# Kernel tuning notes

Measured on AMD Instinct MI355X. Metric: run time of the kernel, lower is better.

Reference implementation:

```python
import jax, jax.numpy as jnp
import numpy as np

D = 1024
HS = 64
NH = D // HS


def setup_inputs() -> dict:
    key = jax.random.key(0)
    ks = jax.random.split(key, 8)
    B, S = 2, 2048
    x = jax.random.normal(ks[0], (B, S, D), dtype=jnp.float32)
    y = jax.random.normal(ks[1], (B, S, D), dtype=jnp.float32)
    pad_mask = jax.random.randint(ks[2], (B, S), 0, 2).astype(jnp.int32)
    sc = 1.0 / np.sqrt(D)
    Wq = jax.random.normal(ks[3], (D, D), dtype=jnp.float32) * sc
    Wk = jax.random.normal(ks[4], (D, D), dtype=jnp.float32) * sc
    Wv = jax.random.normal(ks[5], (D, D), dtype=jnp.float32) * sc
    Wp = jax.random.normal(ks[6], (D, D), dtype=jnp.float32) * sc
    bp = jnp.zeros((D,), dtype=jnp.float32)
    return {"x": x, "y": y, "pad_mask": pad_mask, "Wq": Wq, "Wk": Wk, "Wv": Wv, "Wp": Wp, "bp": bp}


def reference(x, y, pad_mask, Wq, Wk, Wv, Wp, bp):
    B, S, _ = x.shape
    # torch Linear: out = in @ W.T  (bias=False for q/k/v)
    q = (y @ Wq.T).reshape(B, S, NH, HS).transpose(0, 2, 1, 3)  # [B,H,S,hs]
    k = (x @ Wk.T).reshape(B, S, NH, HS).transpose(0, 2, 1, 3)
    v = (x @ Wv.T).reshape(B, S, NH, HS).transpose(0, 2, 1, 3)
    att = jnp.einsum('bhqd,bhkd->bhqk', q, k) * (HS ** -0.5)  # [B,H,S,S]
    att = jnp.where((pad_mask == 0)[:, None, None, :], -jnp.inf, att)
    att = jax.nn.softmax(att, axis=-1)
    out = jnp.einsum('bhqk,bhkd->bhqd', att, v)  # [B,H,S,hs]
    out = out.transpose(0, 2, 1, 3).reshape(B, S, D)
    return out @ Wp.T + bp
```

## Files before the change

kernel.cpp:

```cpp
#include <hip/hip_runtime.h>
#include <hip/hip_bf16.h>
#include <stdint.h>

typedef unsigned short u16;
typedef unsigned int u32;
typedef float __attribute__((ext_vector_type(4))) f32x4;
typedef __bf16 __attribute__((ext_vector_type(8))) bfrag;

#define DEV static __device__ __forceinline__

DEV u16 f2bf(float f) {
  union { float f; u32 u; } c; c.f = f;
  u32 u = c.u;
  u += 0x7fffu + ((u >> 16) & 1u);
  return (u16)(u >> 16);
}

DEV u16 bf16bits(float f) {
  __hip_bfloat16 h = __float2bfloat16(f);
  return *reinterpret_cast<u16*>(&h);
}

typedef const u32 __attribute__((address_space(1)))* gas_t;
typedef u32 __attribute__((address_space(3)))* las_t;

DEV void async16(const void* g, void* l) {
  __builtin_amdgcn_global_load_lds((gas_t)(uintptr_t)g, (las_t)(uintptr_t)l, 16, 0, 0);
}

__global__ __launch_bounds__(256) void convert_all(
    const float* __restrict__ x, const float* __restrict__ y,
    const float* __restrict__ wq, const float* __restrict__ wk,
    const float* __restrict__ wv, const float* __restrict__ wp,
    u16* __restrict__ xb, u16* __restrict__ yb,
    u16* __restrict__ wqb, u16* __restrict__ wkb,
    u16* __restrict__ wvb, u16* __restrict__ wpb) {
  const int NX4 = (2 * 2048 * 1024) / 4;
  const int NW4 = (1024 * 1024) / 4;
  const int total = 2 * NX4 + 4 * NW4;
  for (int i = blockIdx.x * blockDim.x + threadIdx.x; i < total;
       i += gridDim.x * blockDim.x) {
    const float4* s; ushort4* d; int off;
    if (i < NX4) { s = (const float4*)x; d = (ushort4*)xb; off = i; }
    else if (i < 2 * NX4) { s = (const float4*)y; d = (ushort4*)yb; off = i - NX4; }
    else {
      int k = i - 2 * NX4; int wsel = k >> 18; off = k & (NW4 - 1);
      s = (const float4*)(wsel == 0 ? wq : wsel == 1 ? wk : wsel == 2 ? wv : wp);
      d = (ushort4*)(wsel == 0 ? wqb : wsel == 1 ? wkb : wsel == 2 ? wvb : wpb);
    }
    float4 v = s[off];
    ushort4 o; o.x = f2bf(v.x); o.y = f2bf(v.y); o.z = f2bf(v.z); o.w = f2bf(v.w);
    d[off] = o;
  }
}

__global__ __launch_bounds__(256, 3) void gemm_qkv(
    const u16* __restrict__ xb, const u16* __restrict__ yb,
    const u16* __restrict__ wqb, const u16* __restrict__ wkb,
    const u16* __restrict__ wvb,
    u16* __restrict__ Qb, u16* __restrict__ Kb2, u16* __restrict__ Vtb) {
  const int Kd = 1024, Nd = 1024;
  __shared__ __align__(16) u16 Als[128 * 32];
  __shared__ __align__(16) u16 Bls[128 * 32];
  __shared__ __align__(16) u16 Tls[4][64 * 72];

  const int gid = blockIdx.x;
  const int seg = gid >> 8;
  const int bb = gid & 255;
  const int m0 = (bb >> 3) * 128, n0 = (bb & 7) * 128;
  const u16* A  = (seg == 0) ? yb : xb;
  const u16* Bw = (seg == 0) ? wqb : (seg == 1 ? wkb : wvb);

  const int t = threadIdx.x;
  const int lane = t & 63, w = t >> 6;
  const int wr = w >> 1, wc = w & 1;
  const int r15 = lane & 15, g = lane >> 4;
  const int rs = t >> 2, sg = t & 3;

  f32x4 acc[4][4] = {{}};
  const u16* ga = A + (size_t)(m0 + rs) * Kd + sg * 8;
  const u16* gb = Bw + (size_t)(n0 + rs) * Kd + sg * 8;

  for (int k0 = 0; k0 < Kd; k0 += 32) {
    async16(ga + k0, &Als[t * 8]);
    async16(ga + 64 * Kd + k0, &Als[(t + 256) * 8]);
    async16(gb + k0, &Bls[t * 8]);
    async16(gb + 64 * Kd + k0, &Bls[(t + 256) * 8]);
    __syncthreads();
    bfrag af[4], bfr[4];
#pragma unroll
    for (int i = 0; i < 4; i++)
      af[i] = *(const bfrag*)&Als[(wr * 64 + i * 16 + r15) * 32 + g * 8];
#pragma unroll
    for (int i = 0; i < 4; i++)
      bfr[i] = *(const bfrag*)&Bls[(wc * 64 + i * 16 + r15) * 32 + g * 8];
#pragma unroll
    for (int i = 0; i < 4; i++)
#pragma unroll
      for (int j = 0; j < 4; j++)
        acc[i][j] = __builtin_amdgcn_mfma_f32_16x16x32_bf16(af[i], bfr[j], acc[i][j], 0, 0, 0);
    __syncthreads();
  }

  if (seg < 2) {
    u16* C = (seg == 0) ? Qb : Kb2;
    const float scale = (seg == 0) ? 0.125f : 1.0f;
#pragma unroll
    for (int i = 0; i < 4; i++) {
#pragma unroll
      for (int j = 0; j < 4; j++) {
        int col = n0 + wc * 64 + j * 16 + r15;
        int row = m0 + wr * 64 + i * 16 + g * 4;
#pragma unroll
        for (int r = 0; r < 4; r++)
          C[(size_t)(row + r) * Nd + col] = f2bf(acc[i][j][r] * scale);
      }
    }
  } else {
#pragma unroll
    for (int i = 0; i < 4; i++)
#pragma unroll
      for (int j = 0; j < 4; j++)
#pragma unroll
        for (int r = 0; r < 4; r++)
          Tls[w][(j * 16 + r15) * 72 + (i * 16 + g * 4 + r)] = f2bf(acc[i][j][r]);
#pragma unroll
    for (int it = 0; it < 8; ++it) {
      int slot = lane + it * 64;
      int nl = slot >> 3, sgm = slot & 7;
      int4 vrow = *(const int4*)&Tls[w][nl * 72 + sgm * 8];
      int col = n0 + wc * 64 + nl;
      int h = col >> 6, hs = col & 63;
      int rowg = m0 + wr * 64 + sgm * 8;
      int b = rowg >> 11, s = rowg & 2047;
      *(int4*)&Vtb[(((size_t)b * 16 + h) * 64 + hs) * 2048 + s] = vrow;
    }
  }
}

__global__ __launch_bounds__(256, 3) void gemm_proj(
    const u16* __restrict__ A, const u16* __restrict__ Bw,
    float* __restrict__ C, const float* __restrict__ bias) {
  const int Kd = 1024, Nd = 1024;
  __shared__ __align__(16) u16 Als[128 * 32];
  __shared__ __align__(16) u16 Bls[128 * 32];
  const int t = threadIdx.x;
  const int lane = t & 63, w = t >> 6;
  const int wr = w >> 1, wc = w & 1;
  const int r15 = lane & 15, g = lane >> 4;
  const int m0 = blockIdx.y * 128, n0 = blockIdx.x * 128;
  const int rs = t >> 2, sg = t & 3;

  f32x4 acc[4][4] = {{}};
  const u16* ga = A + (size_t)(m0 + rs) * Kd + sg * 8;
  const u16* gb = Bw + (size_t)(n0 + rs) * Kd + sg * 8;

  for (int k0 = 0; k0 < Kd; k0 += 32) {
    async16(ga + k0, &Als[t * 8]);
    async16(ga + 64 * Kd + k0, &Als[(t + 256) * 8]);
    async16(gb + k0, &Bls[t * 8]);
    async16(gb + 64 * Kd + k0, &Bls[(t + 256) * 8]);
    __syncthreads();
    bfrag af[4], bfr[4];
#pragma unroll
    for (int i = 0; i < 4; i++)
      af[i] = *(const bfrag*)&Als[(wr * 64 + i * 16 + r15) * 32 + g * 8];
#pragma unroll
    for (int i = 0; i < 4; i++)
      bfr[i] = *(const bfrag*)&Bls[(wc * 64 + i * 16 + r15) * 32 + g * 8];
#pragma unroll
    for (int i = 0; i < 4; i++)
#pragma unroll
      for (int j = 0; j < 4; j++)
        acc[i][j] = __builtin_amdgcn_mfma_f32_16x16x32_bf16(af[i], bfr[j], acc[i][j], 0, 0, 0);
    __syncthreads();
  }

#pragma unroll
  for (int i = 0; i < 4; i++) {
#pragma unroll
    for (int j = 0; j < 4; j++) {
      int col = n0 + wc * 64 + j * 16 + r15;
      int row = m0 + wr * 64 + i * 16 + g * 4;
      float bv = bias[col];
#pragma unroll
      for (int r = 0; r < 4; r++)
        C[(size_t)(row + r) * Nd + col] = acc[i][j][r] + bv;
    }
  }
}

__global__ __launch_bounds__(256, 4) void attn_fwd(
    const u16* __restrict__ Q, const u16* __restrict__ Kb,
    const u16* __restrict__ Vt, const int* __restrict__ mask,
    u16* __restrict__ O) {
  __shared__ __align__(16) u16 Kls[64 * 64];
  __shared__ __align__(16) u16 Vls[64 * 64];
  __shared__ __align__(16) u16 Pls[4][16 * 64];
  __shared__ float biasl[64];

  const int bid = blockIdx.x;
  const int swz = (bid & 7) * 128 + (bid >> 3);
  const int qblk = swz & 31, bh = swz >> 5;
  const int b = bh >> 4, h = bh & 15;
  const int t = threadIdx.x, lane = t & 63, w = t >> 6;
  const int r15 = lane & 15, g = lane >> 4;
  const int qbase = qblk * 64 + w * 16;

  bfrag aQ[2];
  {
    const u16* Qg = Q + ((size_t)b * 2048 + qbase) * 1024 + h * 64;
#pragma unroll
    for (int ks = 0; ks < 2; ++ks)
      aQ[ks] = *(const bfrag*)&Qg[(size_t)r15 * 1024 + ks * 32 + g * 8];
  }

  f32x4 oacc[4] = {{}};
  float lrow[4] = {0.f, 0.f, 0.f, 0.f};

  const u16* Kg = Kb + (size_t)b * 2048 * 1024 + h * 64;
  const u16* Vg = Vt + (size_t)bh * 64 * 2048;
  const int* mg = mask + b * 2048;

  const int kr = t >> 2, kc = (t & 3) * 16;
  const int swr = (kr & 7) << 3;
  const int rdx = (r15 & 7) << 3;
  int4 nk0, nk1, nv0, nv1; float nbias = 0.f;

  auto stage_load = [&](int kv0) {
    nk0 = *(const int4*)&Kg[(size_t)(kv0 + kr) * 1024 + kc];
    nk1 = *(const int4*)&Kg[(size_t)(kv0 + kr) * 1024 + kc + 8];
    nv0 = *(const int4*)&Vg[(size_t)kr * 2048 + kv0 + kc];
    nv1 = *(const int4*)&Vg[(size_t)kr * 2048 + kv0 + kc + 8];
    if (t < 64) nbias = mg[kv0 + t] ? 0.f : -1e30f;
  };
  auto stage_write = [&]() {
    *(int4*)&Kls[kr * 64 + (kc ^ swr)] = nk0;
    *(int4*)&Kls[kr * 64 + ((kc + 8) ^ swr)] = nk1;
    *(int4*)&Vls[kr * 64 + (kc ^ swr)] = nv0;
    *(int4*)&Vls[kr * 64 + ((kc + 8) ^ swr)] = nv1;
    if (t < 64) biasl[t] = nbias;
  };

  stage_load(0);
  stage_write();
  __syncthreads();

  for (int kt = 0; kt < 32; ++kt) {
    if (kt < 31) stage_load((kt + 1) * 64);

    f32x4 sc[4] = {{}};
#pragma unroll
    for (int ks = 0; ks < 2; ++ks) {
      const int cb = (ks * 32 + g * 8) ^ rdx;
#pragma unroll
      for (int nf = 0; nf < 4; ++nf) {
        bfrag bK = *(const bfrag*)&Kls[(nf * 16 + r15) * 64 + cb];
        sc[nf] = __builtin_amdgcn_mfma_f32_16x16x32_bf16(aQ[ks], bK, sc[nf], 0, 0, 0);
      }
    }

    float bcol[4];
#pragma unroll
    for (int nf = 0; nf < 4; ++nf) bcol[nf] = biasl[nf * 16 + r15];

#pragma unroll
    for (int i = 0; i < 4; i++) {
      const int prow = g * 4 + i;
      const int pxr = (prow & 7) << 3;
      u16* pr = &Pls[w][prow * 64];
      float s = 0.f;
#pragma unroll
      for (int nf = 0; nf < 4; ++nf) {
        float p = __expf(sc[nf][i] + bcol[nf]);
        s += p;
        pr[(nf * 16 + r15) ^ pxr] = bf16bits(p);
      }
      lrow[i] += s;
    }

#pragma unroll
    for (int ks = 0; ks < 2; ++ks) {
      const int cb = (ks * 32 + g * 8) ^ rdx;
      bfrag aP = *(const bfrag*)&Pls[w][r15 * 64 + cb];
#pragma unroll
      for (int nf = 0; nf < 4; ++nf) {
        bfrag bV = *(const bfrag*)&Vls[(nf * 16 + r15) * 64 + cb];
        oacc[nf] = __builtin_amdgcn_mfma_f32_16x16x32_bf16(aP, bV, oacc[nf], 0, 0, 0);
      }
    }

    __syncthreads();
    if (kt < 31) {
      stage_write();
      __syncthreads();
    }
  }

#pragma unroll
  for (int i = 0; i < 4; i++) {
    float s = lrow[i];
    s += __shfl_xor(s, 1);
    s += __shfl_xor(s, 2);
    s += __shfl_xor(s, 4);
    s += __shfl_xor(s, 8);
    lrow[i] = s;
  }

  u16* Og = O + ((size_t)b * 2048 + qbase) * 1024 + h * 64;
#pragma unroll
  for (int i = 0; i < 4; i++) {
    float rl = 1.f / lrow[i];
    size_t ro = (size_t)(g * 4 + i) * 1024;
#pragma unroll
    for (int nf = 0; nf < 4; ++nf)
      Og[ro + nf * 16 + r15] = f2bf(oacc[nf][i] * rl);
  }
}

extern "C" void kernel_launch(void* const* d_in, const int* in_sizes, int n_in,
                              void* d_out, int out_size, void* d_ws, size_t ws_size,
                              hipStream_t stream) {
  const float* x  = (const float*)d_in[0];
  const float* y  = (const float*)d_in[1];
  const int*  msk = (const int*)d_in[2];
  const float* Wq = (const float*)d_in[3];
  const float* Wk = (const float*)d_in[4];
  const float* Wv = (const float*)d_in[5];
  const float* Wp = (const float*)d_in[6];
  const float* bp = (const float*)d_in[7];

  char* ws = (char*)d_ws;
  const size_t SZ_XB = (size_t)2 * 2048 * 1024 * 2;
  const size_t SZ_W  = (size_t)1024 * 1024 * 2;
  u16* xb  = (u16*)(ws);
  u16* yb  = (u16*)(ws + SZ_XB);
  u16* wqb = (u16*)(ws + 2 * SZ_XB);
  u16* wkb = (u16*)(ws + 2 * SZ_XB + SZ_W);
  u16* wvb = (u16*)(ws + 2 * SZ_XB + 2 * SZ_W);
  u16* wpb = (u16*)(ws + 2 * SZ_XB + 3 * SZ_W);
  u16* Qb  = (u16*)(ws + 2 * SZ_XB + 4 * SZ_W);
  u16* Kb2 = (u16*)(ws + 3 * SZ_XB + 4 * SZ_W);
  u16* Vtb = (u16*)(ws + 4 * SZ_XB + 4 * SZ_W);
  u16* Ob  = (u16*)(ws + 5 * SZ_XB + 4 * SZ_W);

  convert_all<<<2048, 256, 0, stream>>>(x, y, Wq, Wk, Wv, Wp, xb, yb, wqb, wkb, wvb, wpb);
  gemm_qkv<<<768, 256, 0, stream>>>(xb, yb, wqb, wkb, wvb, Qb, Kb2, Vtb);
  attn_fwd<<<1024, 256, 0, stream>>>(Qb, Kb2, Vtb, msk, Ob);
  dim3 gg(8, 32);
  gemm_proj<<<gg, 256, 0, stream>>>(Ob, wpb, (float*)d_out, bp);
}
```

Before: 138.1 us.

## Process 32 query rows per wave and compute row sums via MFMA

Each wave in the attention kernel now handles two 16-row query fragments (128 queries per block), so every K/V tile loaded into shared memory is reused across twice as many queries and the grid halves to 512 blocks. The softmax row sum is now accumulated by an extra MFMA of the bf16 P fragment against a vector of ones, replacing the scalar adds and cross-lane shuffle reduction. The cost is more registers (launch bounds lowered to 2 blocks per SM), a larger P buffer in LDS, fewer blocks to fill the GPU, and a row sum taken from bf16-rounded probabilities.

```diff
diff --git a/kernel.cpp b/kernel.cpp
--- a/kernel.cpp
+++ b/kernel.cpp
@@ -6,6 +6,7 @@
 typedef unsigned int u32;
 typedef float __attribute__((ext_vector_type(4))) f32x4;
 typedef __bf16 __attribute__((ext_vector_type(8))) bfrag;
+typedef u16 __attribute__((ext_vector_type(8))) u16x8;
 
 #define DEV static __device__ __forceinline__
 
@@ -190,33 +191,41 @@
   }
 }
 
-__global__ __launch_bounds__(256, 4) void attn_fwd(
+__global__ __launch_bounds__(256, 2) void attn_fwd(
     const u16* __restrict__ Q, const u16* __restrict__ Kb,
     const u16* __restrict__ Vt, const int* __restrict__ mask,
     u16* __restrict__ O) {
   __shared__ __align__(16) u16 Kls[64 * 64];
   __shared__ __align__(16) u16 Vls[64 * 64];
-  __shared__ __align__(16) u16 Pls[4][16 * 64];
+  __shared__ __align__(16) u16 Pls[4][32 * 64];
   __shared__ float biasl[64];
 
   const int bid = blockIdx.x;
-  const int swz = (bid & 7) * 128 + (bid >> 3);
-  const int qblk = swz & 31, bh = swz >> 5;
+  const int swz = (bid & 7) * 64 + (bid >> 3);
+  const int qblk = swz & 15, bh = swz >> 4;
   const int b = bh >> 4, h = bh & 15;
   const int t = threadIdx.x, lane = t & 63, w = t >> 6;
   const int r15 = lane & 15, g = lane >> 4;
-  const int qbase = qblk * 64 + w * 16;
-
-  bfrag aQ[2];
+  const int qbase = qblk * 128 + w * 32;
+
+  bfrag aQ[2][2];
   {
     const u16* Qg = Q + ((size_t)b * 2048 + qbase) * 1024 + h * 64;
 #pragma unroll
-    for (int ks = 0; ks < 2; ++ks)
-      aQ[ks] = *(const bfrag*)&Qg[(size_t)r15 * 1024 + ks * 32 + g * 8];
-  }
-
-  f32x4 oacc[4] = {{}};
-  float lrow[4] = {0.f, 0.f, 0.f, 0.f};
+    for (int mf = 0; mf < 2; ++mf)
+#pragma unroll
+      for (int ks = 0; ks < 2; ++ks)
+        aQ[mf][ks] = *(const bfrag*)&Qg[(size_t)(mf * 16 + r15) * 1024 + ks * 32 + g * 8];
+  }
+
+  bfrag ones;
+  {
+    u16x8 ob = {0x3F80, 0x3F80, 0x3F80, 0x3F80, 0x3F80, 0x3F80, 0x3F80, 0x3F80};
+    ones = *(bfrag*)&ob;
+  }
+
+  f32x4 oacc[2][4] = {};
+  f32x4 osum[2] = {};
 
   const u16* Kg = Kb + (size_t)b * 2048 * 1024 + h * 64;
   const u16* Vg = Vt + (size_t)bh * 64 * 2048;
@@ -249,14 +258,16 @@
   for (int kt = 0; kt < 32; ++kt) {
     if (kt < 31) stage_load((kt + 1) * 64);
 
-    f32x4 sc[4] = {{}};
+    f32x4 sc[2][4] = {};
 #pragma unroll
     for (int ks = 0; ks < 2; ++ks) {
       const int cb = (ks * 32 + g * 8) ^ rdx;
 #pragma unroll
       for (int nf = 0; nf < 4; ++nf) {
         bfrag bK = *(const bfrag*)&Kls[(nf * 16 + r15) * 64 + cb];
-        sc[nf] = __builtin_amdgcn_mfma_f32_16x16x32_bf16(aQ[ks], bK, sc[nf], 0, 0, 0);
+#pragma unroll
+        for (int mf = 0; mf < 2; ++mf)
+          sc[mf][nf] = __builtin_amdgcn_mfma_f32_16x16x32_bf16(aQ[mf][ks], bK, sc[mf][nf], 0, 0, 0);
       }
     }
 
@@ -265,29 +276,36 @@
     for (int nf = 0; nf < 4; ++nf) bcol[nf] = biasl[nf * 16 + r15];
 
 #pragma unroll
-    for (int i = 0; i < 4; i++) {
-      const int prow = g * 4 + i;
-      const int pxr = (prow & 7) << 3;
-      u16* pr = &Pls[w][prow * 64];
-      float s = 0.f;
-#pragma unroll
-      for (int nf = 0; nf < 4; ++nf) {
-        float p = __expf(sc[nf][i] + bcol[nf]);
-        s += p;
-        pr[(nf * 16 + r15) ^ pxr] = bf16bits(p);
+    for (int mf = 0; mf < 2; ++mf)
+#pragma unroll
+      for (int i = 0; i < 4; i++) {
+        const int prow = mf * 16 + g * 4 + i;
+        const int pxr = (prow & 7) << 3;
+        u16* pr = &Pls[w][prow * 64];
+#pragma unroll
+        for (int nf = 0; nf < 4; ++nf) {
+          float p = __expf(sc[mf][nf][i] + bcol[nf]);
+          pr[(nf * 16 + r15) ^ pxr] = bf16bits(p);
+        }
       }
-      lrow[i] += s;
-    }
 
 #pragma unroll
     for (int ks = 0; ks < 2; ++ks) {
       const int cb = (ks * 32 + g * 8) ^ rdx;
-      bfrag aP = *(const bfrag*)&Pls[w][r15 * 64 + cb];
+      bfrag aP[2];
+#pragma unroll
+      for (int mf = 0; mf < 2; ++mf)
+        aP[mf] = *(const bfrag*)&Pls[w][(mf * 16 + r15) * 64 + cb];
 #pragma unroll
       for (int nf = 0; nf < 4; ++nf) {
         bfrag bV = *(const bfrag*)&Vls[(nf * 16 + r15) * 64 + cb];
-        oacc[nf] = __builtin_amdgcn_mfma_f32_16x16x32_bf16(aP, bV, oacc[nf], 0, 0, 0);
+#pragma unroll
+        for (int mf = 0; mf < 2; ++mf)
+          oacc[mf][nf] = __builtin_amdgcn_mfma_f32_16x16x32_bf16(aP[mf], bV, oacc[mf][nf], 0, 0, 0);
       }
+#pragma unroll
+      for (int mf = 0; mf < 2; ++mf)
+        osum[mf] = __builtin_amdgcn_mfma_f32_16x16x32_bf16(aP[mf], ones, osum[mf], 0, 0, 0);
     }
 
     __syncthreads();
@@ -297,25 +315,17 @@
     }
   }
 
-#pragma unroll
-  for (int i = 0; i < 4; i++) {
-    float s = lrow[i];
-    s += __shfl_xor(s, 1);
-    s += __shfl_xor(s, 2);
-    s += __shfl_xor(s, 4);
-    s += __shfl_xor(s, 8);
-    lrow[i] = s;
-  }
-
   u16* Og = O + ((size_t)b * 2048 + qbase) * 1024 + h * 64;
 #pragma unroll
-  for (int i = 0; i < 4; i++) {
-    float rl = 1.f / lrow[i];
-    size_t ro = (size_t)(g * 4 + i) * 1024;
-#pragma unroll
-    for (int nf = 0; nf < 4; ++nf)
-      Og[ro + nf * 16 + r15] = f2bf(oacc[nf][i] * rl);
-  }
+  for (int mf = 0; mf < 2; ++mf)
+#pragma unroll
+    for (int i = 0; i < 4; i++) {
+      float rl = 1.f / osum[mf][i];
+      size_t ro = (size_t)(mf * 16 + g * 4 + i) * 1024;
+#pragma unroll
+      for (int nf = 0; nf < 4; ++nf)
+        Og[ro + nf * 16 + r15] = f2bf(oacc[mf][nf][i] * rl);
+    }
 }
 
 extern "C" void kernel_launch(void* const* d_in, const int* in_sizes, int n_in,
@@ -346,7 +356,7 @@
 
   convert_all<<<2048, 256, 0, stream>>>(x, y, Wq, Wk, Wv, Wp, xb, yb, wqb, wkb, wvb, wpb);
   gemm_qkv<<<768, 256, 0, stream>>>(xb, yb, wqb, wkb, wvb, Qb, Kb2, Vtb);
-  attn_fwd<<<1024, 256, 0, stream>>>(Qb, Kb2, Vtb, msk, Ob);
+  attn_fwd<<<512, 256, 0, stream>>>(Qb, Kb2, Vtb, msk, Ob);
   dim3 gg(8, 32);
   gemm_proj<<<gg, 256, 0, stream>>>(Ob, wpb, (float*)d_out, bp);
 }
```

New measurement: 135.7 us. No clear change (-1.7%).
